# Performance work log

Hardware: AMD Instinct MI355X
Metric: run time of the kernel (lower is better)

## Reference

```python
import jax, jax.numpy as jnp
import numpy as np
import math

D = 768      # embedding_dim
H = 12       # attn_n_heads
HD = D // H  # head_dim = 64
F = 3072     # ff_latent_dim
B, S = 1, 4096
EPS = 1e-5


def setup_inputs() -> dict:
    key = jax.random.key(0)
    ks = jax.random.split(key, 16)
    s = 0.02
    return {
        "x": jax.random.normal(ks[0], (B, S, D), jnp.float32),
        # per-head Q/K/V projections stacked: [H, D, HD]
        "Wq": jax.random.normal(ks[1], (H, D, HD), jnp.float32) * s,
        "bq": jnp.zeros((H, HD), jnp.float32),
        "Wk": jax.random.normal(ks[2], (H, D, HD), jnp.float32) * s,
        "bk": jnp.zeros((H, HD), jnp.float32),
        "Wv": jax.random.normal(ks[3], (H, D, HD), jnp.float32) * s,
        "bv": jnp.zeros((H, HD), jnp.float32),
        "Wo": jax.random.normal(ks[4], (D, D), jnp.float32) * s,
        "bo": jnp.zeros((D,), jnp.float32),
        "ln1_w": jnp.ones((D,), jnp.float32),
        "ln1_b": jnp.zeros((D,), jnp.float32),
        "ln2_w": jnp.ones((D,), jnp.float32),
        "ln2_b": jnp.zeros((D,), jnp.float32),
        "W1": jax.random.normal(ks[5], (D, F), jnp.float32) * s,
        "b1": jnp.zeros((F,), jnp.float32),
        "W2": jax.random.normal(ks[6], (F, D), jnp.float32) * s,
        "b2": jnp.zeros((D,), jnp.float32),
    }


def _layer_norm(z, w, b):
    mu = jnp.mean(z, axis=-1, keepdims=True)
    var = jnp.mean(jnp.square(z - mu), axis=-1, keepdims=True)
    return (z - mu) * jax.lax.rsqrt(var + EPS) * w + b


def reference(x, Wq, bq, Wk, bk, Wv, bv, Wo, bo,
              ln1_w, ln1_b, ln2_w, ln2_b, W1, b1, W2, b2):
    # pre-norm attention block
    y = _layer_norm(x, ln1_w, ln1_b)
    q = jnp.einsum('bsd,hde->bhse', y, Wq) + bq[None, :, None, :]
    k = jnp.einsum('bsd,hde->bhse', y, Wk) + bk[None, :, None, :]
    v = jnp.einsum('bsd,hde->bhse', y, Wv) + bv[None, :, None, :]
    scores = jnp.einsum('bhqe,bhke->bhqk', q, k) * (1.0 / math.sqrt(HD))
    attn = jax.nn.softmax(scores, axis=-1)            # [B,H,S,S]
    o = jnp.einsum('bhqk,bhke->bhqe', attn, v)        # [B,H,S,HD]
    o = o.transpose(0, 2, 1, 3).reshape(x.shape[0], x.shape[1], D)  # concat heads
    o = o @ Wo + bo
    x = x + o
    # pre-norm FFN block (eval mode: dropout is identity)
    y = _layer_norm(x, ln2_w, ln2_b)
    h = jax.nn.gelu(y @ W1 + b1, approximate=False)   # torch F.gelu default = exact erf
    x = x + (h @ W2 + b2)
    return x
```

## Files before the change

kernel.cpp:

```cpp
#include <hip/hip_runtime.h>
#include <stdint.h>

typedef __bf16 bf16;
typedef __bf16 bf16x2 __attribute__((ext_vector_type(2)));
typedef __bf16 bf16x4 __attribute__((ext_vector_type(4)));
typedef __bf16 bf16x8 __attribute__((ext_vector_type(8)));
typedef float f32x4 __attribute__((ext_vector_type(4)));
typedef float f32x16 __attribute__((ext_vector_type(16)));
typedef uint32_t u32;

#define QSCALE 0.1803368801111137f

__device__ __forceinline__ float fast_exp2(float x) {
#if __has_builtin(__builtin_amdgcn_exp2f)
  return __builtin_amdgcn_exp2f(x);
#else
  return exp2f(x);
#endif
}

__device__ __forceinline__ u32 pack_bf16(float a, float b) {
  bf16x2 v; v[0] = (bf16)a; v[1] = (bf16)b;
  return __builtin_bit_cast(u32, v);
}

__device__ __forceinline__ void async16(void* lds, const void* g) {
  __builtin_amdgcn_global_load_lds(
      (__attribute__((address_space(1))) uint32_t*)(uintptr_t)g,
      (__attribute__((address_space(3))) uint32_t*)(uint32_t)(uintptr_t)lds,
      16, 0, 0);
}

__global__ __launch_bounds__(256) void conv_qkv_w_kernel(
    const float* __restrict__ Wq, const float* __restrict__ Wk,
    const float* __restrict__ Wv, bf16* __restrict__ out)
{
  __shared__ float tile[32][33];
  int z = blockIdx.z;
  int part = z / 12, h = z - part * 12;
  const float* W = (part == 0) ? Wq : (part == 1) ? Wk : Wv;
  float sc = (part == 0) ? QSCALE : 1.0f;
  int bd = blockIdx.x * 32, be = blockIdx.y * 32;
  int tc = threadIdx.x & 31, tr = threadIdx.x >> 5;
  #pragma unroll
  for (int i = 0; i < 4; i++)
    tile[tr + i * 8][tc] = W[((size_t)h * 768 + bd + tr + i * 8) * 64 + be + tc] * sc;
  __syncthreads();
  #pragma unroll
  for (int i = 0; i < 4; i++) {
    int e = be + tr + i * 8;
    out[(size_t)(part * 768 + h * 64 + e) * 768 + bd + tc] = (bf16)tile[tc][tr + i * 8];
  }
}

__global__ __launch_bounds__(256) void conv_qkv_b_kernel(
    const float* __restrict__ bq, const float* __restrict__ bk,
    const float* __restrict__ bv, float* __restrict__ out)
{
  int n = blockIdx.x * 256 + threadIdx.x;
  int part = n / 768, nn = n - part * 768;
  const float* B = (part == 0) ? bq : (part == 1) ? bk : bv;
  float v = B[nn];
  if (part == 0) v *= QSCALE;
  out[n] = v;
}

__global__ __launch_bounds__(256) void transpose_tile_kernel(
    const float* __restrict__ in, bf16* __restrict__ out, int R, int C)
{
  __shared__ float tile[32][33];
  int bc = blockIdx.x * 32, br = blockIdx.y * 32;
  int tc = threadIdx.x & 31, tr = threadIdx.x >> 5;
  #pragma unroll
  for (int i = 0; i < 4; i++)
    tile[tr + i * 8][tc] = in[(size_t)(br + tr + i * 8) * C + bc + tc];
  __syncthreads();
  #pragma unroll
  for (int i = 0; i < 4; i++) {
    int c = bc + tr + i * 8;
    out[(size_t)c * R + br + tc] = (bf16)tile[tc][tr + i * 8];
  }
}

__global__ __launch_bounds__(256) void reduce_add_kernel(
    float* __restrict__ out, const bf16* __restrict__ p)
{
  int i = blockIdx.x * 256 + threadIdx.x;
  float4 o = ((float4*)out)[i];
  bf16x4 v = ((const bf16x4*)p)[i];
  o.x += (float)v[0]; o.y += (float)v[1];
  o.z += (float)v[2]; o.w += (float)v[3];
  ((float4*)out)[i] = o;
}

__global__ __launch_bounds__(256) void ln_kernel(
    const float* __restrict__ x, const float* __restrict__ w,
    const float* __restrict__ b, bf16* __restrict__ y)
{
  int row = blockIdx.x;
  const float* xr = x + (size_t)row * 768;
  int t = threadIdx.x;
  float v0 = xr[t], v1 = xr[t + 256], v2 = xr[t + 512];
  float s = v0 + v1 + v2, s2 = v0 * v0 + v1 * v1 + v2 * v2;
  #pragma unroll
  for (int d = 1; d < 64; d <<= 1) {
    s  += __shfl_xor(s, d, 64);
    s2 += __shfl_xor(s2, d, 64);
  }
  __shared__ float red[8];
  int wv = t >> 6, ln = t & 63;
  if (ln == 0) { red[wv] = s; red[4 + wv] = s2; }
  __syncthreads();
  s  = red[0] + red[1] + red[2] + red[3];
  s2 = red[4] + red[5] + red[6] + red[7];
  float mu = s * (1.0f / 768.0f);
  float var = s2 * (1.0f / 768.0f) - mu * mu;
  float rstd = rsqrtf(var + 1e-5f);
  bf16* yr = y + (size_t)row * 768;
  yr[t]       = (bf16)((v0 - mu) * rstd * w[t]       + b[t]);
  yr[t + 256] = (bf16)((v1 - mu) * rstd * w[t + 256] + b[t + 256]);
  yr[t + 512] = (bf16)((v2 - mu) * rstd * w[t + 512] + b[t + 512]);
}

template <int MODE>
__global__ __launch_bounds__(256) void gemm_bt(
    const bf16* __restrict__ A, const bf16* __restrict__ Bt,
    const float* __restrict__ bias, const float* __restrict__ res,
    void* __restrict__ outp, void* __restrict__ out2, int M, int N, int K)
{
  __shared__ bf16 As[128 * 32];
  __shared__ bf16 Bs[128 * 32];
  int t = threadIdx.x;
  int w = t >> 6, lane = t & 63;
  int quad = lane >> 4, l16 = lane & 15;
  int tile_m = blockIdx.y * 128, tile_n = blockIdx.x * 128;

  int srow = lane >> 2;
  int skb = (lane & 3) * 8;
  const bf16* Ag = A  + (size_t)(tile_m + w * 16 + srow) * K + skb;
  const bf16* Bg = Bt + (size_t)(tile_n + w * 16 + srow) * K + skb;
  char* AsB = (char*)As + w * 1024;
  char* BsB = (char*)Bs + w * 1024;
  size_t rstep = (size_t)64 * K;

  int wm = (w >> 1) * 64, wn = (w & 1) * 64;
  f32x4 acc[4][4] = {};

  int kbeg = 0, kend = K;
  if (MODE == 5) {
    int half = K >> 1;
    kbeg = blockIdx.z * half;
    kend = kbeg + half;
  }

  for (int k0 = kbeg; k0 < kend; k0 += 32) {
    __syncthreads();
    async16(AsB,        Ag + k0);
    async16(AsB + 4096, Ag + rstep + k0);
    async16(BsB,        Bg + k0);
    async16(BsB + 4096, Bg + rstep + k0);
    __syncthreads();

    bf16x8 af[4], bfr[4];
    #pragma unroll
    for (int mb = 0; mb < 4; mb++)
      af[mb] = *(const bf16x8*)(As + (wm + mb * 16 + l16) * 32 + quad * 8);
    #pragma unroll
    for (int nb = 0; nb < 4; nb++)
      bfr[nb] = *(const bf16x8*)(Bs + (wn + nb * 16 + l16) * 32 + quad * 8);
    #pragma unroll
    for (int mb = 0; mb < 4; mb++)
      #pragma unroll
      for (int nb = 0; nb < 4; nb++)
        acc[mb][nb] = __builtin_amdgcn_mfma_f32_16x16x32_bf16(
            af[mb], bfr[nb], acc[mb][nb], 0, 0, 0);
  }

  #pragma unroll
  for (int mb = 0; mb < 4; mb++) {
    #pragma unroll
    for (int nb = 0; nb < 4; nb++) {
      int col = tile_n + wn + nb * 16 + l16;
      int row0 = tile_m + wm + mb * 16 + quad * 4;
      if (MODE == 4) {
        float bc = bias[col];
        if (col < 1536) {
          #pragma unroll
          for (int r = 0; r < 4; r++)
            ((bf16*)outp)[(size_t)(row0 + r) * 1536 + col] =
                (bf16)(acc[mb][nb][r] + bc);
        } else {
          bf16x4 pk;
          #pragma unroll
          for (int r = 0; r < 4; r++) pk[r] = (bf16)(acc[mb][nb][r] + bc);
          *(bf16x4*)((bf16*)out2 + (size_t)(col - 1536) * 4096 + row0) = pk;
        }
      } else if (MODE == 2) {
        float bc = bias[col];
        #pragma unroll
        for (int r = 0; r < 4; r++) {
          size_t idx = (size_t)(row0 + r) * N + col;
          float v = acc[mb][nb][r] + bc;
          float g = 0.5f * v * (1.0f + erff(v * 0.70710678118654752f));
          ((bf16*)outp)[idx] = (bf16)g;
        }
      } else {
        if (blockIdx.z == 0) {
          float bc = bias[col];
          #pragma unroll
          for (int r = 0; r < 4; r++) {
            size_t idx = (size_t)(row0 + r) * N + col;
            ((float*)outp)[idx] = res[idx] + acc[mb][nb][r] + bc;
          }
        } else {
          #pragma unroll
          for (int r = 0; r < 4; r++) {
            size_t idx = (size_t)(row0 + r) * N + col;
            ((bf16*)out2)[idx] = (bf16)acc[mb][nb][r];
          }
        }
      }
    }
  }
}

__global__ __launch_bounds__(256) void flash_kernel(
    const bf16* __restrict__ qk, const bf16* __restrict__ vtg,
    bf16* __restrict__ Opart, float* __restrict__ Lpart)
{
  __shared__ char smem[24576];
  bf16* Qs = (bf16*)smem;
  bf16* Ks = (bf16*)(smem + 8192);
  bf16* Vs = (bf16*)(smem + 16384);
  int t = threadIdx.x, w = t >> 6, lane = t & 63;
  int l32 = lane & 31, hi = lane >> 5;
  int qt = blockIdx.x, h = blockIdx.y, z = blockIdx.z;
  int q0 = qt * 64, kv0 = z * 2048;
  int qsel = w & 1, ksel = w >> 1;
  int qb = qsel * 32, kb = ksel * 32;

  int srow = lane >> 3, scol = ((lane & 7) ^ srow) * 8;

  {
    const bf16* qg = qk + (size_t)(q0 + w * 8 + srow) * 1536 + h * 64 + scol;
    char* base = smem + w * 1024;
    async16(base,        qg);
    async16(base + 4096, qg + (size_t)32 * 1536);
  }
  __syncthreads();

  int qrow = qb + l32;
  bf16x8 qf[4];
  #pragma unroll
  for (int ks = 0; ks < 4; ks++) {
    int pos = (ks * 2 + hi) ^ (qrow & 7);
    qf[ks] = *(const bf16x8*)(Qs + qrow * 64 + pos * 8);
  }

  const bf16* kg = qk + 768 + h * 64 + (size_t)(kv0 + w * 8 + srow) * 1536 + scol;
  const bf16* vg = vtg + (size_t)(h * 64 + w * 8 + srow) * 4096 + kv0 + scol;

  f32x16 oT0 = {}, oT1 = {};
  float l_lane = 0.0f;
  int krow = kb + l32;
  int erow0 = l32, erow1 = 32 + l32;

  for (int j = 0; j < 32; j++) {
    __syncthreads();
    {
      char* base = smem + 8192 + w * 1024;
      async16(base,        kg);
      async16(base + 4096, kg + (size_t)32 * 1536);
    }
    {
      char* base = smem + 16384 + w * 1024;
      async16(base,        vg);
      async16(base + 4096, vg + (size_t)32 * 4096);
    }
    kg += (size_t)64 * 1536;
    vg += 64;
    __syncthreads();

    f32x16 sT = {};
    #pragma unroll
    for (int ks = 0; ks < 4; ks++) {
      int pos = (ks * 2 + hi) ^ (krow & 7);
      bf16x8 kf = *(const bf16x8*)(Ks + krow * 64 + pos * 8);
      sT = __builtin_amdgcn_mfma_f32_32x32x16_bf16(kf, qf[ks], sT, 0, 0, 0);
    }

    float rs = 0.0f;
    #pragma unroll
    for (int i = 0; i < 16; i++) {
      float p = fast_exp2(sT[i]);
      sT[i] = p;
      rs += p;
    }
    l_lane += rs;

    u32 dd[8], xx[8];
    #pragma unroll
    for (int k = 0; k < 8; k++) dd[k] = pack_bf16(sT[2 * k], sT[2 * k + 1]);
    #pragma unroll
    for (int k = 0; k < 8; k++) xx[k] = __shfl_xor((int)dd[k], 32, 64);
    uint4 p0 = hi ? uint4{xx[2], xx[3], dd[2], dd[3]}
                  : uint4{dd[0], dd[1], xx[0], xx[1]};
    uint4 p1 = hi ? uint4{xx[6], xx[7], dd[6], dd[7]}
                  : uint4{dd[4], dd[5], xx[4], xx[5]};
    bf16x8 pf0 = __builtin_bit_cast(bf16x8, p0);
    bf16x8 pf1 = __builtin_bit_cast(bf16x8, p1);

    #pragma unroll
    for (int ks = 0; ks < 2; ks++) {
      int grp = (kb >> 3) + ks * 2 + hi;
      bf16x8 pf  = ks ? pf1 : pf0;
      bf16x8 vf0 = *(const bf16x8*)(Vs + erow0 * 64 + (grp ^ (erow0 & 7)) * 8);
      bf16x8 vf1 = *(const bf16x8*)(Vs + erow1 * 64 + (grp ^ (erow1 & 7)) * 8);
      oT0 = __builtin_amdgcn_mfma_f32_32x32x16_bf16(vf0, pf, oT0, 0, 0, 0);
      oT1 = __builtin_amdgcn_mfma_f32_32x32x16_bf16(vf1, pf, oT1, 0, 0, 0);
    }
  }

  float l_q = l_lane + __shfl_xor(l_lane, 32, 64);
  __syncthreads();
  float* OS = (float*)smem;
  float* LS = (float*)(smem + 17408);
  if (ksel == 1) {
    #pragma unroll
    for (int i = 0; i < 16; i++) {
      int e0 = (i & 3) + 8 * (i >> 2) + 4 * hi;
      OS[qrow * 68 + e0]      = oT0[i];
      OS[qrow * 68 + 32 + e0] = oT1[i];
    }
    if (hi == 0) LS[qrow] = l_q;
  }
  __syncthreads();
  if (ksel == 0) {
    size_t tbase = ((size_t)z * 12 + h) * 64 + qt;
    float lall = l_q + LS[qrow];
    if (hi == 0) Lpart[tbase * 64 + qrow] = lall;
    bf16* ob = Opart + tbase * 4096 + (size_t)qrow * 64;
    #pragma unroll
    for (int g = 0; g < 4; g++) {
      int e0 = 8 * g + 4 * hi;
      bf16x4 pk0, pk1;
      #pragma unroll
      for (int r = 0; r < 4; r++) {
        pk0[r] = (bf16)(oT0[g * 4 + r] + OS[qrow * 68 + e0 + r]);
        pk1[r] = (bf16)(oT1[g * 4 + r] + OS[qrow * 68 + 32 + e0 + r]);
      }
      *(bf16x4*)(ob + e0)      = pk0;
      *(bf16x4*)(ob + 32 + e0) = pk1;
    }
  }
}

__global__ __launch_bounds__(256) void flash_combine_kernel(
    const bf16* __restrict__ Opart, const float* __restrict__ Lpart,
    bf16* __restrict__ o)
{
  int qt = blockIdx.x, h = blockIdx.y;
  int t = threadIdx.x;
  int q = t >> 2, eg = (t & 3) * 16;
  size_t t0 = (size_t)h * 64 + qt;
  size_t t1 = (size_t)(12 + h) * 64 + qt;
  float inv = 1.0f / (Lpart[t0 * 64 + q] + Lpart[t1 * 64 + q]);
  const bf16* p0 = Opart + t0 * 4096 + q * 64 + eg;
  const bf16* p1 = Opart + t1 * 4096 + q * 64 + eg;
  bf16x8 a0 = *(const bf16x8*)p0, a1 = *(const bf16x8*)(p0 + 8);
  bf16x8 b0 = *(const bf16x8*)p1, b1 = *(const bf16x8*)(p1 + 8);
  bf16x8 r0, r1;
  #pragma unroll
  for (int i = 0; i < 8; i++) {
    r0[i] = (bf16)(((float)a0[i] + (float)b0[i]) * inv);
    r1[i] = (bf16)(((float)a1[i] + (float)b1[i]) * inv);
  }
  bf16* op = o + (size_t)(qt * 64 + q) * 768 + h * 64 + eg;
  *(bf16x8*)op       = r0;
  *(bf16x8*)(op + 8) = r1;
}

extern "C" void kernel_launch(void* const* d_in, const int* in_sizes, int n_in,
                              void* d_out, int out_size, void* d_ws, size_t ws_size,
                              hipStream_t stream) {
  const float* x    = (const float*)d_in[0];
  const float* Wq   = (const float*)d_in[1];
  const float* bq   = (const float*)d_in[2];
  const float* Wk   = (const float*)d_in[3];
  const float* bk   = (const float*)d_in[4];
  const float* Wv   = (const float*)d_in[5];
  const float* bv   = (const float*)d_in[6];
  const float* Wo   = (const float*)d_in[7];
  const float* bo   = (const float*)d_in[8];
  const float* ln1w = (const float*)d_in[9];
  const float* ln1b = (const float*)d_in[10];
  const float* ln2w = (const float*)d_in[11];
  const float* ln2b = (const float*)d_in[12];
  const float* W1   = (const float*)d_in[13];
  const float* b1   = (const float*)d_in[14];
  const float* W2   = (const float*)d_in[15];
  const float* b2   = (const float*)d_in[16];
  float* out = (float*)d_out;

  char* ws = (char*)d_ws;
  bf16*  hbuf   = (bf16*)(ws + 0);
  float* Lpart  = (float*)(ws + 0);
  bf16*  ybuf   = (bf16*)(ws + 0);
  bf16*  qkbuf  = (bf16*)(ws + 6291456);
  bf16*  opar_o = (bf16*)(ws + 6291456);
  bf16*  vtg    = (bf16*)(ws + 18874368);
  float* x1     = (float*)(ws + 25165824);
  bf16*  Opart  = (bf16*)(ws + 25165824);
  bf16*  obuf   = (bf16*)(ws + 37748736);
  bf16*  y2buf  = obuf;
  bf16*  opar_f = obuf;
  bf16*  Wqkv_t = (bf16*)(ws + 44040192);
  bf16*  Wo_t   = (bf16*)(ws + 47579136);
  bf16*  W1_t   = (bf16*)(ws + 48758784);
  bf16*  W2_t   = (bf16*)(ws + 53477376);
  float* bqkv   = (float*)(ws + 58195968);

  conv_qkv_w_kernel<<<dim3(24, 2, 36), 256, 0, stream>>>(Wq, Wk, Wv, Wqkv_t);
  conv_qkv_b_kernel<<<9, 256, 0, stream>>>(bq, bk, bv, bqkv);
  transpose_tile_kernel<<<dim3(24, 24), 256, 0, stream>>>(Wo, Wo_t, 768, 768);
  transpose_tile_kernel<<<dim3(96, 24), 256, 0, stream>>>(W1, W1_t, 768, 3072);
  transpose_tile_kernel<<<dim3(24, 96), 256, 0, stream>>>(W2, W2_t, 3072, 768);

  ln_kernel<<<4096, 256, 0, stream>>>(x, ln1w, ln1b, ybuf);
  gemm_bt<4><<<dim3(18, 32), 256, 0, stream>>>(ybuf, Wqkv_t, bqkv,
                                               (const float*)nullptr, qkbuf, vtg,
                                               4096, 2304, 768);
  flash_kernel<<<dim3(64, 12, 2), 256, 0, stream>>>(qkbuf, vtg, Opart, Lpart);
  flash_combine_kernel<<<dim3(64, 12), 256, 0, stream>>>(Opart, Lpart, obuf);
  gemm_bt<5><<<dim3(6, 32, 2), 256, 0, stream>>>(obuf, Wo_t, bo, x, x1, opar_o,
                                                 4096, 768, 768);
  reduce_add_kernel<<<3072, 256, 0, stream>>>(x1, opar_o);
  ln_kernel<<<4096, 256, 0, stream>>>(x1, ln2w, ln2b, y2buf);
  gemm_bt<2><<<dim3(24, 32), 256, 0, stream>>>(y2buf, W1_t, b1,
                                               (const float*)nullptr, hbuf, nullptr,
                                               4096, 3072, 768);
  gemm_bt<5><<<dim3(6, 32, 2), 256, 0, stream>>>(hbuf, W2_t, b2, x1, out, opar_f,
                                                 4096, 768, 3072);
  reduce_add_kernel<<<3072, 256, 0, stream>>>(out, opar_f);
}
```

Before: 356.4 us.

## Double-buffer K/V tiles and drop KV split with combine kernel

The flash attention kernel now processes the full 4096-key range per block instead of splitting keys across two blocks. This removes the separate combine kernel and the partial output/LSE buffers, and normalization is folded into the epilogue. K/V tiles are double-buffered in LDS so the next tile's async loads overlap the current tile's compute, with one barrier per iteration. The trade-off is half as many blocks, a longer serial loop per block, and larger LDS use per block.

```diff
diff --git a/kernel.cpp b/kernel.cpp
--- a/kernel.cpp
+++ b/kernel.cpp
@@ -226,16 +226,14 @@
 
 __global__ __launch_bounds__(256) void flash_kernel(
     const bf16* __restrict__ qk, const bf16* __restrict__ vtg,
-    bf16* __restrict__ Opart, float* __restrict__ Lpart)
-{
-  __shared__ char smem[24576];
+    bf16* __restrict__ o)
+{
+  __shared__ char smem[40960];
   bf16* Qs = (bf16*)smem;
-  bf16* Ks = (bf16*)(smem + 8192);
-  bf16* Vs = (bf16*)(smem + 16384);
   int t = threadIdx.x, w = t >> 6, lane = t & 63;
   int l32 = lane & 31, hi = lane >> 5;
-  int qt = blockIdx.x, h = blockIdx.y, z = blockIdx.z;
-  int q0 = qt * 64, kv0 = z * 2048;
+  int qt = blockIdx.x, h = blockIdx.y;
+  int q0 = qt * 64;
   int qsel = w & 1, ksel = w >> 1;
   int qb = qsel * 32, kb = ksel * 32;
 
@@ -247,6 +245,18 @@
     async16(base,        qg);
     async16(base + 4096, qg + (size_t)32 * 1536);
   }
+
+  const bf16* kg = qk + 768 + h * 64 + (size_t)(w * 8 + srow) * 1536 + scol;
+  const bf16* vg = vtg + (size_t)(h * 64 + w * 8 + srow) * 4096 + scol;
+
+  {
+    char* kb0 = smem + 8192  + w * 1024;
+    char* vb0 = smem + 24576 + w * 1024;
+    async16(kb0,        kg);
+    async16(kb0 + 4096, kg + (size_t)32 * 1536);
+    async16(vb0,        vg);
+    async16(vb0 + 4096, vg + (size_t)32 * 4096);
+  }
   __syncthreads();
 
   int qrow = qb + l32;
@@ -256,30 +266,26 @@
     int pos = (ks * 2 + hi) ^ (qrow & 7);
     qf[ks] = *(const bf16x8*)(Qs + qrow * 64 + pos * 8);
   }
-
-  const bf16* kg = qk + 768 + h * 64 + (size_t)(kv0 + w * 8 + srow) * 1536 + scol;
-  const bf16* vg = vtg + (size_t)(h * 64 + w * 8 + srow) * 4096 + kv0 + scol;
 
   f32x16 oT0 = {}, oT1 = {};
   float l_lane = 0.0f;
   int krow = kb + l32;
   int erow0 = l32, erow1 = 32 + l32;
 
-  for (int j = 0; j < 32; j++) {
-    __syncthreads();
-    {
-      char* base = smem + 8192 + w * 1024;
-      async16(base,        kg);
-      async16(base + 4096, kg + (size_t)32 * 1536);
-    }
-    {
-      char* base = smem + 16384 + w * 1024;
-      async16(base,        vg);
-      async16(base + 4096, vg + (size_t)32 * 4096);
-    }
-    kg += (size_t)64 * 1536;
-    vg += 64;
-    __syncthreads();
+  for (int j = 0; j < 64; j++) {
+    int cur = j & 1;
+    if (j < 63) {
+      const bf16* kgn = kg + (size_t)(j + 1) * 64 * 1536;
+      const bf16* vgn = vg + (j + 1) * 64;
+      char* kbn = smem + 8192  + (cur ^ 1) * 8192 + w * 1024;
+      char* vbn = smem + 24576 + (cur ^ 1) * 8192 + w * 1024;
+      async16(kbn,        kgn);
+      async16(kbn + 4096, kgn + (size_t)32 * 1536);
+      async16(vbn,        vgn);
+      async16(vbn + 4096, vgn + (size_t)32 * 4096);
+    }
+    const bf16* Ks = (const bf16*)(smem + 8192  + cur * 8192);
+    const bf16* Vs = (const bf16*)(smem + 24576 + cur * 8192);
 
     f32x16 sT = {};
     #pragma unroll
@@ -319,10 +325,11 @@
       oT0 = __builtin_amdgcn_mfma_f32_32x32x16_bf16(vf0, pf, oT0, 0, 0, 0);
       oT1 = __builtin_amdgcn_mfma_f32_32x32x16_bf16(vf1, pf, oT1, 0, 0, 0);
     }
+
+    __syncthreads();
   }
 
   float l_q = l_lane + __shfl_xor(l_lane, 32, 64);
-  __syncthreads();
   float* OS = (float*)smem;
   float* LS = (float*)(smem + 17408);
   if (ksel == 1) {
@@ -336,48 +343,21 @@
   }
   __syncthreads();
   if (ksel == 0) {
-    size_t tbase = ((size_t)z * 12 + h) * 64 + qt;
-    float lall = l_q + LS[qrow];
-    if (hi == 0) Lpart[tbase * 64 + qrow] = lall;
-    bf16* ob = Opart + tbase * 4096 + (size_t)qrow * 64;
+    float inv = 1.0f / (l_q + LS[qrow]);
+    bf16* ob = o + (size_t)(q0 + qrow) * 768 + h * 64;
     #pragma unroll
     for (int g = 0; g < 4; g++) {
       int e0 = 8 * g + 4 * hi;
       bf16x4 pk0, pk1;
       #pragma unroll
       for (int r = 0; r < 4; r++) {
-        pk0[r] = (bf16)(oT0[g * 4 + r] + OS[qrow * 68 + e0 + r]);
-        pk1[r] = (bf16)(oT1[g * 4 + r] + OS[qrow * 68 + 32 + e0 + r]);
+        pk0[r] = (bf16)((oT0[g * 4 + r] + OS[qrow * 68 + e0 + r]) * inv);
+        pk1[r] = (bf16)((oT1[g * 4 + r] + OS[qrow * 68 + 32 + e0 + r]) * inv);
       }
       *(bf16x4*)(ob + e0)      = pk0;
       *(bf16x4*)(ob + 32 + e0) = pk1;
     }
   }
-}
-
-__global__ __launch_bounds__(256) void flash_combine_kernel(
-    const bf16* __restrict__ Opart, const float* __restrict__ Lpart,
-    bf16* __restrict__ o)
-{
-  int qt = blockIdx.x, h = blockIdx.y;
-  int t = threadIdx.x;
-  int q = t >> 2, eg = (t & 3) * 16;
-  size_t t0 = (size_t)h * 64 + qt;
-  size_t t1 = (size_t)(12 + h) * 64 + qt;
-  float inv = 1.0f / (Lpart[t0 * 64 + q] + Lpart[t1 * 64 + q]);
-  const bf16* p0 = Opart + t0 * 4096 + q * 64 + eg;
-  const bf16* p1 = Opart + t1 * 4096 + q * 64 + eg;
-  bf16x8 a0 = *(const bf16x8*)p0, a1 = *(const bf16x8*)(p0 + 8);
-  bf16x8 b0 = *(const bf16x8*)p1, b1 = *(const bf16x8*)(p1 + 8);
-  bf16x8 r0, r1;
-  #pragma unroll
-  for (int i = 0; i < 8; i++) {
-    r0[i] = (bf16)(((float)a0[i] + (float)b0[i]) * inv);
-    r1[i] = (bf16)(((float)a1[i] + (float)b1[i]) * inv);
-  }
-  bf16* op = o + (size_t)(qt * 64 + q) * 768 + h * 64 + eg;
-  *(bf16x8*)op       = r0;
-  *(bf16x8*)(op + 8) = r1;
 }
 
 extern "C" void kernel_launch(void* const* d_in, const int* in_sizes, int n_in,
@@ -404,13 +384,11 @@
 
   char* ws = (char*)d_ws;
   bf16*  hbuf   = (bf16*)(ws + 0);
-  float* Lpart  = (float*)(ws + 0);
   bf16*  ybuf   = (bf16*)(ws + 0);
   bf16*  qkbuf  = (bf16*)(ws + 6291456);
   bf16*  opar_o = (bf16*)(ws + 6291456);
   bf16*  vtg    = (bf16*)(ws + 18874368);
   float* x1     = (float*)(ws + 25165824);
-  bf16*  Opart  = (bf16*)(ws + 25165824);
   bf16*  obuf   = (bf16*)(ws + 37748736);
   bf16*  y2buf  = obuf;
   bf16*  opar_f = obuf;
@@ -430,8 +408,7 @@
   gemm_bt<4><<<dim3(18, 32), 256, 0, stream>>>(ybuf, Wqkv_t, bqkv,
                                                (const float*)nullptr, qkbuf, vtg,
                                                4096, 2304, 768);
-  flash_kernel<<<dim3(64, 12, 2), 256, 0, stream>>>(qkbuf, vtg, Opart, Lpart);
-  flash_combine_kernel<<<dim3(64, 12), 256, 0, stream>>>(Opart, Lpart, obuf);
+  flash_kernel<<<dim3(64, 12), 256, 0, stream>>>(qkbuf, vtg, obuf);
   gemm_bt<5><<<dim3(6, 32, 2), 256, 0, stream>>>(obuf, Wo_t, bo, x, x1, opar_o,
                                                  4096, 768, 768);
   reduce_add_kernel<<<3072, 256, 0, stream>>>(x1, opar_o);
```

Result: no change. 356.9 us (+0.1%).

## Double-buffer K/V in flash attention, widen Q tile, fuse residual add into LN2

Applied to the files above, without the earlier changes.

The flash kernel now gives each block 128 query rows, so each wave handles 64 rows against a shared K/V tile, doubling reuse of each loaded K/V tile. K/V loads are double-buffered in LDS so the next tile's async copy overlaps the current tile's MFMA work, and one barrier per iteration is removed. The residual reduce_add and the second layer norm are fused into a single ln_add kernel, saving a launch and one pass over x1. The cost is twice the LDS (48KB) and more accumulator registers per wave, which may lower occupancy, and half as many flash blocks (768 instead of 1536).

```diff
diff --git a/kernel.cpp b/kernel.cpp
--- a/kernel.cpp
+++ b/kernel.cpp
@@ -101,6 +101,40 @@
   const float* xr = x + (size_t)row * 768;
   int t = threadIdx.x;
   float v0 = xr[t], v1 = xr[t + 256], v2 = xr[t + 512];
+  float s = v0 + v1 + v2, s2 = v0 * v0 + v1 * v1 + v2 * v2;
+  #pragma unroll
+  for (int d = 1; d < 64; d <<= 1) {
+    s  += __shfl_xor(s, d, 64);
+    s2 += __shfl_xor(s2, d, 64);
+  }
+  __shared__ float red[8];
+  int wv = t >> 6, ln = t & 63;
+  if (ln == 0) { red[wv] = s; red[4 + wv] = s2; }
+  __syncthreads();
+  s  = red[0] + red[1] + red[2] + red[3];
+  s2 = red[4] + red[5] + red[6] + red[7];
+  float mu = s * (1.0f / 768.0f);
+  float var = s2 * (1.0f / 768.0f) - mu * mu;
+  float rstd = rsqrtf(var + 1e-5f);
+  bf16* yr = y + (size_t)row * 768;
+  yr[t]       = (bf16)((v0 - mu) * rstd * w[t]       + b[t]);
+  yr[t + 256] = (bf16)((v1 - mu) * rstd * w[t + 256] + b[t + 256]);
+  yr[t + 512] = (bf16)((v2 - mu) * rstd * w[t + 512] + b[t + 512]);
+}
+
+__global__ __launch_bounds__(256) void ln_add_kernel(
+    float* __restrict__ x1, const bf16* __restrict__ p,
+    const float* __restrict__ w, const float* __restrict__ b,
+    bf16* __restrict__ y)
+{
+  int row = blockIdx.x;
+  float* xr = x1 + (size_t)row * 768;
+  const bf16* pr = p + (size_t)row * 768;
+  int t = threadIdx.x;
+  float v0 = xr[t]       + (float)pr[t];
+  float v1 = xr[t + 256] + (float)pr[t + 256];
+  float v2 = xr[t + 512] + (float)pr[t + 512];
+  xr[t] = v0; xr[t + 256] = v1; xr[t + 512] = v2;
   float s = v0 + v1 + v2, s2 = v0 * v0 + v1 * v1 + v2 * v2;
   #pragma unroll
   for (int d = 1; d < 64; d <<= 1) {
@@ -228,129 +262,157 @@
     const bf16* __restrict__ qk, const bf16* __restrict__ vtg,
     bf16* __restrict__ Opart, float* __restrict__ Lpart)
 {
-  __shared__ char smem[24576];
+  __shared__ char smem[49152];
   bf16* Qs = (bf16*)smem;
-  bf16* Ks = (bf16*)(smem + 8192);
-  bf16* Vs = (bf16*)(smem + 16384);
   int t = threadIdx.x, w = t >> 6, lane = t & 63;
   int l32 = lane & 31, hi = lane >> 5;
   int qt = blockIdx.x, h = blockIdx.y, z = blockIdx.z;
-  int q0 = qt * 64, kv0 = z * 2048;
+  int q0 = qt * 128, kv0 = z * 2048;
   int qsel = w & 1, ksel = w >> 1;
-  int qb = qsel * 32, kb = ksel * 32;
+  int qw = qsel * 64, kb = ksel * 32;
 
   int srow = lane >> 3, scol = ((lane & 7) ^ srow) * 8;
 
-  {
-    const bf16* qg = qk + (size_t)(q0 + w * 8 + srow) * 1536 + h * 64 + scol;
-    char* base = smem + w * 1024;
-    async16(base,        qg);
-    async16(base + 4096, qg + (size_t)32 * 1536);
-  }
-  __syncthreads();
-
-  int qrow = qb + l32;
-  bf16x8 qf[4];
-  #pragma unroll
-  for (int ks = 0; ks < 4; ks++) {
-    int pos = (ks * 2 + hi) ^ (qrow & 7);
-    qf[ks] = *(const bf16x8*)(Qs + qrow * 64 + pos * 8);
+  #pragma unroll
+  for (int c = 0; c < 4; c++) {
+    const bf16* qg = qk + (size_t)(q0 + c * 32 + w * 8 + srow) * 1536 + h * 64 + scol;
+    async16(smem + c * 4096 + w * 1024, qg);
   }
 
   const bf16* kg = qk + 768 + h * 64 + (size_t)(kv0 + w * 8 + srow) * 1536 + scol;
   const bf16* vg = vtg + (size_t)(h * 64 + w * 8 + srow) * 4096 + kv0 + scol;
 
-  f32x16 oT0 = {}, oT1 = {};
-  float l_lane = 0.0f;
+  {
+    char* kb0 = smem + 16384 + w * 1024;
+    char* vb0 = smem + 32768 + w * 1024;
+    async16(kb0,        kg);
+    async16(kb0 + 4096, kg + (size_t)32 * 1536);
+    async16(vb0,        vg);
+    async16(vb0 + 4096, vg + (size_t)32 * 4096);
+  }
+  __syncthreads();
+
+  int qr0 = qw + l32, qr1 = qw + 32 + l32;
+  bf16x8 qf0[4], qf1[4];
+  #pragma unroll
+  for (int ks = 0; ks < 4; ks++) {
+    qf0[ks] = *(const bf16x8*)(Qs + qr0 * 64 + (((ks * 2 + hi) ^ (qr0 & 7)) * 8));
+    qf1[ks] = *(const bf16x8*)(Qs + qr1 * 64 + (((ks * 2 + hi) ^ (qr1 & 7)) * 8));
+  }
+
+  f32x16 oT00 = {}, oT10 = {}, oT01 = {}, oT11 = {};
+  float l0 = 0.0f, l1 = 0.0f;
   int krow = kb + l32;
-  int erow0 = l32, erow1 = 32 + l32;
+  int er0 = l32, er1 = 32 + l32;
 
   for (int j = 0; j < 32; j++) {
+    int cur = j & 1;
+    if (j < 31) {
+      const bf16* kgn = kg + (size_t)(j + 1) * 64 * 1536;
+      const bf16* vgn = vg + (j + 1) * 64;
+      char* kbn = smem + 16384 + (cur ^ 1) * 8192 + w * 1024;
+      char* vbn = smem + 32768 + (cur ^ 1) * 8192 + w * 1024;
+      async16(kbn,        kgn);
+      async16(kbn + 4096, kgn + (size_t)32 * 1536);
+      async16(vbn,        vgn);
+      async16(vbn + 4096, vgn + (size_t)32 * 4096);
+    }
+    const bf16* Ks = (const bf16*)(smem + 16384 + cur * 8192);
+    const bf16* Vs = (const bf16*)(smem + 32768 + cur * 8192);
+
+    f32x16 s0 = {}, s1 = {};
+    #pragma unroll
+    for (int ks = 0; ks < 4; ks++) {
+      bf16x8 kf = *(const bf16x8*)(Ks + krow * 64 + (((ks * 2 + hi) ^ (krow & 7)) * 8));
+      s0 = __builtin_amdgcn_mfma_f32_32x32x16_bf16(kf, qf0[ks], s0, 0, 0, 0);
+      s1 = __builtin_amdgcn_mfma_f32_32x32x16_bf16(kf, qf1[ks], s1, 0, 0, 0);
+    }
+
+    bf16x8 pf00, pf01, pf10, pf11;
+    {
+      float rs = 0.0f;
+      #pragma unroll
+      for (int i = 0; i < 16; i++) { float p = fast_exp2(s0[i]); s0[i] = p; rs += p; }
+      l0 += rs;
+      u32 dd[8], xx[8];
+      #pragma unroll
+      for (int k = 0; k < 8; k++) dd[k] = pack_bf16(s0[2 * k], s0[2 * k + 1]);
+      #pragma unroll
+      for (int k = 0; k < 8; k++) xx[k] = __shfl_xor((int)dd[k], 32, 64);
+      uint4 a = hi ? uint4{xx[2], xx[3], dd[2], dd[3]} : uint4{dd[0], dd[1], xx[0], xx[1]};
+      uint4 b = hi ? uint4{xx[6], xx[7], dd[6], dd[7]} : uint4{dd[4], dd[5], xx[4], xx[5]};
+      pf00 = __builtin_bit_cast(bf16x8, a);
+      pf01 = __builtin_bit_cast(bf16x8, b);
+    }
+    {
+      float rs = 0.0f;
+      #pragma unroll
+      for (int i = 0; i < 16; i++) { float p = fast_exp2(s1[i]); s1[i] = p; rs += p; }
+      l1 += rs;
+      u32 dd[8], xx[8];
+      #pragma unroll
+      for (int k = 0; k < 8; k++) dd[k] = pack_bf16(s1[2 * k], s1[2 * k + 1]);
+      #pragma unroll
+      for (int k = 0; k < 8; k++) xx[k] = __shfl_xor((int)dd[k], 32, 64);
+      uint4 a = hi ? uint4{xx[2], xx[3], dd[2], dd[3]} : uint4{dd[0], dd[1], xx[0], xx[1]};
+      uint4 b = hi ? uint4{xx[6], xx[7], dd[6], dd[7]} : uint4{dd[4], dd[5], xx[4], xx[5]};
+      pf10 = __builtin_bit_cast(bf16x8, a);
+      pf11 = __builtin_bit_cast(bf16x8, b);
+    }
+
+    #pragma unroll
+    for (int kstep = 0; kstep < 2; kstep++) {
+      int grp = (kb >> 3) + kstep * 2 + hi;
+      bf16x8 va = *(const bf16x8*)(Vs + er0 * 64 + ((grp ^ (er0 & 7)) * 8));
+      bf16x8 vb = *(const bf16x8*)(Vs + er1 * 64 + ((grp ^ (er1 & 7)) * 8));
+      bf16x8 pa = kstep ? pf01 : pf00;
+      bf16x8 pb = kstep ? pf11 : pf10;
+      oT00 = __builtin_amdgcn_mfma_f32_32x32x16_bf16(va, pa, oT00, 0, 0, 0);
+      oT10 = __builtin_amdgcn_mfma_f32_32x32x16_bf16(vb, pa, oT10, 0, 0, 0);
+      oT01 = __builtin_amdgcn_mfma_f32_32x32x16_bf16(va, pb, oT01, 0, 0, 0);
+      oT11 = __builtin_amdgcn_mfma_f32_32x32x16_bf16(vb, pb, oT11, 0, 0, 0);
+    }
+
     __syncthreads();
-    {
-      char* base = smem + 8192 + w * 1024;
-      async16(base,        kg);
-      async16(base + 4096, kg + (size_t)32 * 1536);
-    }
-    {
-      char* base = smem + 16384 + w * 1024;
-      async16(base,        vg);
-      async16(base + 4096, vg + (size_t)32 * 4096);
-    }
-    kg += (size_t)64 * 1536;
-    vg += 64;
-    __syncthreads();
-
-    f32x16 sT = {};
-    #pragma unroll
-    for (int ks = 0; ks < 4; ks++) {
-      int pos = (ks * 2 + hi) ^ (krow & 7);
-      bf16x8 kf = *(const bf16x8*)(Ks + krow * 64 + pos * 8);
-      sT = __builtin_amdgcn_mfma_f32_32x32x16_bf16(kf, qf[ks], sT, 0, 0, 0);
-    }
-
-    float rs = 0.0f;
+  }
+
+  float lq0 = l0 + __shfl_xor(l0, 32, 64);
+  float lq1 = l1 + __shfl_xor(l1, 32, 64);
+  float* OS = (float*)smem;
+  float* LS = (float*)(smem + 34304);
+  if (ksel == 1) {
     #pragma unroll
     for (int i = 0; i < 16; i++) {
-      float p = fast_exp2(sT[i]);
-      sT[i] = p;
-      rs += p;
-    }
-    l_lane += rs;
-
-    u32 dd[8], xx[8];
-    #pragma unroll
-    for (int k = 0; k < 8; k++) dd[k] = pack_bf16(sT[2 * k], sT[2 * k + 1]);
-    #pragma unroll
-    for (int k = 0; k < 8; k++) xx[k] = __shfl_xor((int)dd[k], 32, 64);
-    uint4 p0 = hi ? uint4{xx[2], xx[3], dd[2], dd[3]}
-                  : uint4{dd[0], dd[1], xx[0], xx[1]};
-    uint4 p1 = hi ? uint4{xx[6], xx[7], dd[6], dd[7]}
-                  : uint4{dd[4], dd[5], xx[4], xx[5]};
-    bf16x8 pf0 = __builtin_bit_cast(bf16x8, p0);
-    bf16x8 pf1 = __builtin_bit_cast(bf16x8, p1);
-
-    #pragma unroll
-    for (int ks = 0; ks < 2; ks++) {
-      int grp = (kb >> 3) + ks * 2 + hi;
-      bf16x8 pf  = ks ? pf1 : pf0;
-      bf16x8 vf0 = *(const bf16x8*)(Vs + erow0 * 64 + (grp ^ (erow0 & 7)) * 8);
-      bf16x8 vf1 = *(const bf16x8*)(Vs + erow1 * 64 + (grp ^ (erow1 & 7)) * 8);
-      oT0 = __builtin_amdgcn_mfma_f32_32x32x16_bf16(vf0, pf, oT0, 0, 0, 0);
-      oT1 = __builtin_amdgcn_mfma_f32_32x32x16_bf16(vf1, pf, oT1, 0, 0, 0);
-    }
-  }
-
-  float l_q = l_lane + __shfl_xor(l_lane, 32, 64);
-  __syncthreads();
-  float* OS = (float*)smem;
-  float* LS = (float*)(smem + 17408);
-  if (ksel == 1) {
-    #pragma unroll
-    for (int i = 0; i < 16; i++) {
-      int e0 = (i & 3) + 8 * (i >> 2) + 4 * hi;
-      OS[qrow * 68 + e0]      = oT0[i];
-      OS[qrow * 68 + 32 + e0] = oT1[i];
-    }
-    if (hi == 0) LS[qrow] = l_q;
+      int eoff = (i & 3) + 8 * (i >> 2) + 4 * hi;
+      OS[qr0 * 67 + eoff]      = oT00[i];
+      OS[qr0 * 67 + 32 + eoff] = oT10[i];
+      OS[qr1 * 67 + eoff]      = oT01[i];
+      OS[qr1 * 67 + 32 + eoff] = oT11[i];
+    }
+    if (hi == 0) { LS[qr0] = lq0; LS[qr1] = lq1; }
   }
   __syncthreads();
   if (ksel == 0) {
-    size_t tbase = ((size_t)z * 12 + h) * 64 + qt;
-    float lall = l_q + LS[qrow];
-    if (hi == 0) Lpart[tbase * 64 + qrow] = lall;
-    bf16* ob = Opart + tbase * 4096 + (size_t)qrow * 64;
+    size_t tb = ((size_t)z * 12 + h) * 32 + qt;
+    float la0 = lq0 + LS[qr0], la1 = lq1 + LS[qr1];
+    if (hi == 0) { Lpart[tb * 128 + qr0] = la0; Lpart[tb * 128 + qr1] = la1; }
+    bf16* ob0 = Opart + tb * 8192 + (size_t)qr0 * 64;
+    bf16* ob1 = Opart + tb * 8192 + (size_t)qr1 * 64;
     #pragma unroll
     for (int g = 0; g < 4; g++) {
       int e0 = 8 * g + 4 * hi;
-      bf16x4 pk0, pk1;
+      bf16x4 a0, a1, b0, b1;
       #pragma unroll
       for (int r = 0; r < 4; r++) {
-        pk0[r] = (bf16)(oT0[g * 4 + r] + OS[qrow * 68 + e0 + r]);
-        pk1[r] = (bf16)(oT1[g * 4 + r] + OS[qrow * 68 + 32 + e0 + r]);
+        a0[r] = (bf16)(oT00[g * 4 + r] + OS[qr0 * 67 + e0 + r]);
+        a1[r] = (bf16)(oT10[g * 4 + r] + OS[qr0 * 67 + 32 + e0 + r]);
+        b0[r] = (bf16)(oT01[g * 4 + r] + OS[qr1 * 67 + e0 + r]);
+        b1[r] = (bf16)(oT11[g * 4 + r] + OS[qr1 * 67 + 32 + e0 + r]);
       }
-      *(bf16x4*)(ob + e0)      = pk0;
-      *(bf16x4*)(ob + 32 + e0) = pk1;
+      *(bf16x4*)(ob0 + e0)      = a0;
+      *(bf16x4*)(ob0 + 32 + e0) = a1;
+      *(bf16x4*)(ob1 + e0)      = b0;
+      *(bf16x4*)(ob1 + 32 + e0) = b1;
     }
   }
 }
@@ -361,23 +423,26 @@
 {
   int qt = blockIdx.x, h = blockIdx.y;
   int t = threadIdx.x;
-  int q = t >> 2, eg = (t & 3) * 16;
-  size_t t0 = (size_t)h * 64 + qt;
-  size_t t1 = (size_t)(12 + h) * 64 + qt;
-  float inv = 1.0f / (Lpart[t0 * 64 + q] + Lpart[t1 * 64 + q]);
-  const bf16* p0 = Opart + t0 * 4096 + q * 64 + eg;
-  const bf16* p1 = Opart + t1 * 4096 + q * 64 + eg;
-  bf16x8 a0 = *(const bf16x8*)p0, a1 = *(const bf16x8*)(p0 + 8);
-  bf16x8 b0 = *(const bf16x8*)p1, b1 = *(const bf16x8*)(p1 + 8);
-  bf16x8 r0, r1;
-  #pragma unroll
-  for (int i = 0; i < 8; i++) {
-    r0[i] = (bf16)(((float)a0[i] + (float)b0[i]) * inv);
-    r1[i] = (bf16)(((float)a1[i] + (float)b1[i]) * inv);
-  }
-  bf16* op = o + (size_t)(qt * 64 + q) * 768 + h * 64 + eg;
-  *(bf16x8*)op       = r0;
-  *(bf16x8*)(op + 8) = r1;
+  size_t t0 = (size_t)h * 32 + qt;
+  size_t t1 = (size_t)(12 + h) * 32 + qt;
+  #pragma unroll
+  for (int qq = 0; qq < 2; qq++) {
+    int q = qq * 64 + (t >> 2), eg = (t & 3) * 16;
+    float inv = 1.0f / (Lpart[t0 * 128 + q] + Lpart[t1 * 128 + q]);
+    const bf16* p0 = Opart + t0 * 8192 + (size_t)q * 64 + eg;
+    const bf16* p1 = Opart + t1 * 8192 + (size_t)q * 64 + eg;
+    bf16x8 a0 = *(const bf16x8*)p0, a1 = *(const bf16x8*)(p0 + 8);
+    bf16x8 b0 = *(const bf16x8*)p1, b1 = *(const bf16x8*)(p1 + 8);
+    bf16x8 r0, r1;
+    #pragma unroll
+    for (int i = 0; i < 8; i++) {
+      r0[i] = (bf16)(((float)a0[i] + (float)b0[i]) * inv);
+      r1[i] = (bf16)(((float)a1[i] + (float)b1[i]) * inv);
+    }
+    bf16* op = o + (size_t)(qt * 128 + q) * 768 + h * 64 + eg;
+    *(bf16x8*)op       = r0;
+    *(bf16x8*)(op + 8) = r1;
+  }
 }
 
 extern "C" void kernel_launch(void* const* d_in, const int* in_sizes, int n_in,
@@ -430,12 +495,11 @@
   gemm_bt<4><<<dim3(18, 32), 256, 0, stream>>>(ybuf, Wqkv_t, bqkv,
                                                (const float*)nullptr, qkbuf, vtg,
                                                4096, 2304, 768);
-  flash_kernel<<<dim3(64, 12, 2), 256, 0, stream>>>(qkbuf, vtg, Opart, Lpart);
-  flash_combine_kernel<<<dim3(64, 12), 256, 0, stream>>>(Opart, Lpart, obuf);
+  flash_kernel<<<dim3(32, 12, 2), 256, 0, stream>>>(qkbuf, vtg, Opart, Lpart);
+  flash_combine_kernel<<<dim3(32, 12), 256, 0, stream>>>(Opart, Lpart, obuf);
   gemm_bt<5><<<dim3(6, 32, 2), 256, 0, stream>>>(obuf, Wo_t, bo, x, x1, opar_o,
                                                  4096, 768, 768);
-  reduce_add_kernel<<<3072, 256, 0, stream>>>(x1, opar_o);
-  ln_kernel<<<4096, 256, 0, stream>>>(x1, ln2w, ln2b, y2buf);
+  ln_add_kernel<<<4096, 256, 0, stream>>>(x1, opar_o, ln2w, ln2b, y2buf);
   gemm_bt<2><<<dim3(24, 32), 256, 0, stream>>>(y2buf, W1_t, b1,
                                                (const float*)nullptr, hbuf, nullptr,
                                                4096, 3072, 768);
```

Result: no change. 355.0 us (-0.4%).
